# Kernel tuning notes

Hardware: AMD Instinct MI355X
Metric: run time of the kernel (lower is better)

## Reference

```python
import jax, jax.numpy as jnp
import numpy as np

GRID_LON = 17  # idx = lat*17 + lon in original code


def setup_inputs() -> dict:
    key = jax.random.key(0)
    ks = jax.random.split(key, 16)
    B, S, L = 512, 256, 64
    DIM_RHO, DIM_C, HID = 256, 128, 512
    N_LAT, N_LON = 17, GRID_LON

    rho = jax.random.normal(ks[0], (B, S, DIM_RHO), dtype=jnp.float32)
    c = jax.random.normal(ks[1], (1, DIM_C, N_LAT, N_LON), dtype=jnp.float32)
    w = jax.random.uniform(ks[2], (B, S), dtype=jnp.float32, minval=1e-3, maxval=1.0)
    l = jax.random.uniform(ks[3], (B,), dtype=jnp.float32, minval=0.1, maxval=10.0)
    roads = jax.random.randint(ks[4], (B, L), 0, N_LAT * N_LON)
    lon_idx = jax.random.randint(ks[5], (B, L), 0, N_LON)
    lat_idx = jax.random.randint(ks[6], (B, L), 0, N_LAT)

    sc = lambda fan_in: 1.0 / np.sqrt(fan_in)
    # f2: MLP(128, 256, 128) with selu
    f2_W1 = jax.random.uniform(ks[7], (DIM_C, 256), jnp.float32, -sc(DIM_C), sc(DIM_C))
    f2_b1 = jnp.zeros((256,), jnp.float32)
    f2_W2 = jax.random.uniform(ks[8], (256, DIM_C), jnp.float32, -sc(256), sc(256))
    f2_b2 = jnp.zeros((DIM_C,), jnp.float32)
    # f: MLP2(dim_rho + dim_c, hidden, 1) with selu (use_selu=True)
    fin = DIM_RHO + DIM_C
    f_W1 = jax.random.uniform(ks[9], (fin, HID), jnp.float32, -sc(fin), sc(fin))
    f_b1 = jnp.zeros((HID,), jnp.float32)
    f_W21 = jax.random.uniform(ks[10], (HID, 1), jnp.float32, -sc(HID), sc(HID))
    f_b21 = jnp.zeros((1,), jnp.float32)
    f_W22 = jax.random.uniform(ks[11], (HID, 1), jnp.float32, -sc(HID), sc(HID))
    f_b22 = jnp.zeros((1,), jnp.float32)

    return dict(rho=rho, c=c, w=w, l=l, roads=roads, lon_idx=lon_idx,
                lat_idx=lat_idx, f2_W1=f2_W1, f2_b1=f2_b1, f2_W2=f2_W2,
                f2_b2=f2_b2, f_W1=f_W1, f_b1=f_b1, f_W21=f_W21, f_b21=f_b21,
                f_W22=f_W22, f_b22=f_b22)


def reference(rho, c, w, l, roads, lon_idx, lat_idx,
              f2_W1, f2_b1, f2_W2, f2_b2,
              f_W1, f_b1, f_W21, f_b21, f_W22, f_b22):
    # c: (1, dim_c, n_lat, n_lon) -> (n_lat*n_lon, dim_c)
    c3 = jnp.squeeze(c, 0)                       # (dim_c, n_lat, n_lon)
    c_flat = jnp.transpose(c3, (1, 2, 0)).reshape(-1, c3.shape[0])  # (cells, dim_c)

    # ragged gather-mean, vectorized: (B, L) cell indices -> (B, dim_c)
    idx = lat_idx * GRID_LON + lon_idx           # (B, L)
    c_traj = jnp.mean(c_flat[idx], axis=1)       # (B, dim_c)

    # f2: selu MLP (dropout inactive / eval mode)
    h = jax.nn.selu(c_traj @ f2_W1 + f2_b1)
    c_tr = h @ f2_W2 + f2_b2                     # (B, dim_c)

    # broadcast over seq and concat with rho
    S = rho.shape[1]
    c_exp = jnp.broadcast_to(c_tr[:, None, :], (rho.shape[0], S, c_tr.shape[-1]))
    x = jnp.concatenate([rho, c_exp], axis=2)    # (B, S, dim_rho + dim_c)

    # f (MLP2, selu since use_selu=True)
    h1 = jax.nn.selu(x @ f_W1 + f_b1)            # (B, S, hidden)
    logm = (h1 @ f_W21 + f_b21)[..., 0]          # (B, S)
    logv = (h1 @ f_W22 + f_b22)[..., 0]          # (B, S)

    logw = jnp.log(w)
    logm_agg = jax.nn.logsumexp(logm + logw, axis=1)       # (B,)
    logv_agg = jax.nn.logsumexp(logv + 2.0 * logw, axis=1) # (B,)
    logl = jnp.log(l)
    log_mu = logl - logm_agg
    log_lambda = logl - 3.0 * logm_agg - logv_agg
    return (log_mu, log_lambda)
```

## Files before the change

### kernel.cpp

```cpp
#include <hip/hip_runtime.h>
#include <hip/hip_bf16.h>

typedef short bf16x8 __attribute__((ext_vector_type(8)));
typedef float f32x4 __attribute__((ext_vector_type(4)));
typedef _Float16 half4 __attribute__((ext_vector_type(4)));

__device__ __forceinline__ short f2bf(float f) {
    union { float f; unsigned u; } v; v.f = f;
    unsigned r = (v.u + 0x7FFFu + ((v.u >> 16) & 1u)) >> 16;
    return (short)r;
}

__device__ __forceinline__ float selu_f(float x) {
    const float scale = 1.0507009873554805f;
    const float sa = 1.0507009873554805f * 1.6732632423543772f;
    return x > 0.f ? scale * x : sa * (__expf(x) - 1.f);
}

__global__ void __launch_bounds__(512) prep_all_kernel(
    const float* __restrict__ c, const int* __restrict__ lat_idx,
    const int* __restrict__ lon_idx,
    const float* __restrict__ f2W1, const float* __restrict__ f2b1,
    const float* __restrict__ f2W2, const float* __restrict__ f2b2,
    const float* __restrict__ fW1, const float* __restrict__ fb1,
    const float* __restrict__ fW21, const float* __restrict__ fW22,
    short* __restrict__ w1img, _Float16* __restrict__ wvec,
    float* __restrict__ cbias)
{
    const int bid = blockIdx.x;
    const int t = threadIdx.x;

    if (bid < 512) {
        __shared__ int cells[64];
        __shared__ float ctraj[128];
        __shared__ float hbuf[256];
        __shared__ float ctrf[128];
        const int b = bid;

        if (t < 64) cells[t] = lat_idx[b * 64 + t] * 17 + lon_idx[b * 64 + t];
        __syncthreads();

        if (t < 128) {
            float s = 0.f;
            #pragma unroll 8
            for (int j = 0; j < 64; ++j) s += c[t * 289 + cells[j]];
            ctraj[t] = s * (1.f / 64.f);
        }
        __syncthreads();

        if (t < 256) {
            float acc = f2b1[t];
            #pragma unroll 8
            for (int i = 0; i < 128; ++i) acc += ctraj[i] * f2W1[i * 256 + t];
            hbuf[t] = selu_f(acc);
        }
        __syncthreads();

        if (t < 128) {
            float acc = f2b2[t];
            #pragma unroll 8
            for (int i = 0; i < 256; ++i) acc += hbuf[i] * f2W2[i * 128 + t];
            ctrf[t] = acc;
        }
        __syncthreads();

        float acc = fb1[t];
        #pragma unroll 8
        for (int i = 0; i < 128; ++i) acc += ctrf[i] * fW1[(256 + i) * 512 + t];
        cbias[b * 512 + t] = acc;
    } else if (bid < 768) {
        int I = (bid - 512) * 512 + t;
        int e = I & 7;
        int lane = (I >> 3) & 63;
        int cg = (I >> 9) & 31;
        int kc = I >> 14;
        int col = cg * 16 + (lane & 15);
        int k = kc * 32 + ((lane >> 4) << 3) + e;
        w1img[I] = f2bf(fW1[k * 512 + col]);
    } else {
        int I = (bid - 768) * 512 + t;
        int e = I & 3;
        int lane = (I >> 2) & 63;
        int nc = I >> 8;
        int l15 = lane & 15, hi = lane >> 4;
        int n = nc * 16 + hi * 4 + e;
        float v = (l15 == 0) ? fW21[n] : (l15 == 1 ? fW22[n] : 0.f);
        wvec[I] = (_Float16)v;
    }
}

__global__ void __launch_bounds__(512, 4) fused_gemm_kernel(
    const float* __restrict__ rho, const short* __restrict__ w1img,
    const float* __restrict__ cbias, const _Float16* __restrict__ wvec,
    float* __restrict__ plm, float* __restrict__ plv)
{
    __shared__ __align__(16) char smA[36864];

    const int tid  = threadIdx.x;
    const int lane = tid & 63;
    const int w    = tid >> 6;
    const int l15  = lane & 15;
    const int hi   = lane >> 4;

    const int b  = blockIdx.x >> 2;
    const int s0 = (blockIdx.x & 3) << 6;

    {
        const float* src = rho + (size_t)(b * 256 + s0) * 256 + tid * 8;
        const int kc_w = (tid >> 2) & 7;
        const int hi_w = tid & 3;
        const int sw_w = (tid >> 5) ^ (tid & 15);
        #pragma unroll
        for (int j = 0; j < 4; ++j) {
            float4 f0 = *(const float4*)(src + j * 4096);
            float4 f1 = *(const float4*)(src + j * 4096 + 4);
            union { bf16x8 h; unsigned u[4]; } pk;
            asm("v_cvt_pk_bf16_f32 %0, %1, %2" : "=v"(pk.u[0]) : "v"(f0.x), "v"(f0.y));
            asm("v_cvt_pk_bf16_f32 %0, %1, %2" : "=v"(pk.u[1]) : "v"(f0.z), "v"(f0.w));
            asm("v_cvt_pk_bf16_f32 %0, %1, %2" : "=v"(pk.u[2]) : "v"(f1.x), "v"(f1.y));
            asm("v_cvt_pk_bf16_f32 %0, %1, %2" : "=v"(pk.u[3]) : "v"(f1.z), "v"(f1.w));
            int slot = (kc_w * 4 + j) * 64 + hi_w * 16 + sw_w;
            *(bf16x8*)(smA + (slot << 4)) = pk.h;
        }
    }
    __syncthreads();

    f32x4 acc[4][4];
    #pragma unroll
    for (int nf = 0; nf < 4; ++nf)
        #pragma unroll
        for (int sf = 0; sf < 4; ++sf)
            acc[nf][sf] = (f32x4){0.f, 0.f, 0.f, 0.f};

    const char* bp = (const char*)w1img + w * 4096 + lane * 16;

    bf16x8 bN[4];
    #pragma unroll
    for (int nf = 0; nf < 4; ++nf)
        bN[nf] = *(const bf16x8*)(bp + nf * 1024);

    #pragma unroll
    for (int kc = 0; kc < 8; ++kc) {
        bf16x8 bC[4];
        #pragma unroll
        for (int nf = 0; nf < 4; ++nf) bC[nf] = bN[nf];
        if (kc < 7) {
            #pragma unroll
            for (int nf = 0; nf < 4; ++nf)
                bN[nf] = *(const bf16x8*)(bp + (size_t)(kc + 1) * 32768 + nf * 1024);
        }
        const int sw_r = l15 ^ (((kc & 3) << 2) | hi);
        const char* ab = smA + ((kc * 256 + hi * 16 + sw_r) << 4);
        bf16x8 aF[4];
        #pragma unroll
        for (int sf = 0; sf < 4; ++sf)
            aF[sf] = *(const bf16x8*)(ab + sf * 1024);
        #pragma unroll
        for (int nf = 0; nf < 4; ++nf)
            #pragma unroll
            for (int sf = 0; sf < 4; ++sf)
                acc[nf][sf] = __builtin_amdgcn_mfma_f32_16x16x32_bf16(
                    bC[nf], aF[sf], acc[nf][sf], 0, 0, 0);
    }

    f32x4 rd[4];
    #pragma unroll
    for (int sf = 0; sf < 4; ++sf) rd[sf] = (f32x4){0.f, 0.f, 0.f, 0.f};

    #pragma unroll
    for (int nf = 0; nf < 4; ++nf) {
        f32x4 cbf = *(const f32x4*)(cbias + b * 512 + w * 64 + nf * 16 + hi * 4);
        half4 wv = *(const half4*)(wvec + (size_t)(w * 4 + nf) * 256 + lane * 4);
        #pragma unroll
        for (int sf = 0; sf < 4; ++sf) {
            half4 pa;
            #pragma unroll
            for (int q = 0; q < 4; ++q)
                pa[q] = (_Float16)selu_f(acc[nf][sf][q] + cbf[q]);
            rd[sf] = __builtin_amdgcn_mfma_f32_16x16x16f16(pa, wv, rd[sf], 0, 0, 0);
        }
    }

    float* redM = (float*)(smA + 32768);
    float* redV = (float*)(smA + 34816);
    if (l15 == 0) {
        #pragma unroll
        for (int sf = 0; sf < 4; ++sf)
            *(f32x4*)&redM[w * 64 + sf * 16 + hi * 4] = rd[sf];
    } else if (l15 == 1) {
        #pragma unroll
        for (int sf = 0; sf < 4; ++sf)
            *(f32x4*)&redV[w * 64 + sf * 16 + hi * 4] = rd[sf];
    }

    __syncthreads();
    size_t obase = (size_t)b * 256 + s0;
    if (tid < 64) {
        float s = 0.f;
        #pragma unroll
        for (int j = 0; j < 8; ++j) s += redM[j * 64 + tid];
        plm[obase + tid] = s;
    } else if (tid < 128) {
        int rr = tid - 64;
        float s = 0.f;
        #pragma unroll
        for (int j = 0; j < 8; ++j) s += redV[j * 64 + rr];
        plv[obase + rr] = s;
    }
}

__global__ void __launch_bounds__(64) finalize_kernel(
    const float* __restrict__ plm, const float* __restrict__ plv,
    const float* __restrict__ w, const float* __restrict__ l,
    const float* __restrict__ b21p, const float* __restrict__ b22p,
    float* __restrict__ out)
{
    const int b = blockIdx.x;
    const int lane = threadIdx.x;
    const float b21 = b21p[0], b22 = b22p[0];

    float a1[4], a2[4];
    float m1 = -1e30f, m2 = -1e30f;
    #pragma unroll
    for (int i = 0; i < 4; ++i) {
        int s = i * 64 + lane;
        float lw = logf(w[b * 256 + s]);
        a1[i] = plm[b * 256 + s] + b21 + lw;
        a2[i] = plv[b * 256 + s] + b22 + 2.f * lw;
        m1 = fmaxf(m1, a1[i]);
        m2 = fmaxf(m2, a2[i]);
    }
    #pragma unroll
    for (int m = 1; m < 64; m <<= 1) {
        m1 = fmaxf(m1, __shfl_xor(m1, m));
        m2 = fmaxf(m2, __shfl_xor(m2, m));
    }
    float s1 = 0.f, s2 = 0.f;
    #pragma unroll
    for (int i = 0; i < 4; ++i) {
        s1 += expf(a1[i] - m1);
        s2 += expf(a2[i] - m2);
    }
    #pragma unroll
    for (int m = 1; m < 64; m <<= 1) {
        s1 += __shfl_xor(s1, m);
        s2 += __shfl_xor(s2, m);
    }
    if (lane == 0) {
        float lm_agg = m1 + logf(s1);
        float lv_agg = m2 + logf(s2);
        float logl = logf(l[b]);
        out[b]       = logl - lm_agg;
        out[512 + b] = logl - 3.f * lm_agg - lv_agg;
    }
}

extern "C" void kernel_launch(void* const* d_in, const int* in_sizes, int n_in,
                              void* d_out, int out_size, void* d_ws, size_t ws_size,
                              hipStream_t stream) {
    const float* rho     = (const float*)d_in[0];
    const float* c       = (const float*)d_in[1];
    const float* w       = (const float*)d_in[2];
    const float* l       = (const float*)d_in[3];
    const int*   lon_idx = (const int*)d_in[5];
    const int*   lat_idx = (const int*)d_in[6];
    const float* f2W1    = (const float*)d_in[7];
    const float* f2b1    = (const float*)d_in[8];
    const float* f2W2    = (const float*)d_in[9];
    const float* f2b2    = (const float*)d_in[10];
    const float* fW1     = (const float*)d_in[11];
    const float* fb1     = (const float*)d_in[12];
    const float* fW21    = (const float*)d_in[13];
    const float* fb21    = (const float*)d_in[14];
    const float* fW22    = (const float*)d_in[15];
    const float* fb22    = (const float*)d_in[16];
    float* out = (float*)d_out;

    char* ws = (char*)d_ws;
    float*     cbias = (float*)(ws);
    short*     w1img = (short*)(ws + 1048576);
    float*     plm   = (float*)(ws + 1310720);
    float*     plv   = (float*)(ws + 1835008);
    _Float16*  wvec  = (_Float16*)(ws + 2359296);

    prep_all_kernel<<<784, 512, 0, stream>>>(c, lat_idx, lon_idx,
                                             f2W1, f2b1, f2W2, f2b2,
                                             fW1, fb1, fW21, fW22,
                                             w1img, wvec, cbias);
    fused_gemm_kernel<<<2048, 512, 0, stream>>>(rho, w1img, cbias, wvec,
                                                plm, plv);
    finalize_kernel<<<512, 64, 0, stream>>>(plm, plv, w, l, fb21, fb22, out);
}
```

Before: 92.33 us.

## Stream W1 tiles via async global-to-LDS loads with triple buffering

Replaces the per-wave register prefetch of W1 fragments with direct global_load_lds transfers into a per-wave triple-buffered LDS region, issued two k-steps ahead and paced with explicit vmcnt waits. MFMA blocks are wrapped in s_setprio to favour the compute wave. LDS usage grows from 36 KB to 128 KB and launch bounds drop from 4 to 2 blocks per CU, so occupancy falls. The aim is to hide global load latency and free VGPRs, at the cost of extra LDS traffic.

```diff
diff --git a/kernel.cpp b/kernel.cpp
--- a/kernel.cpp
+++ b/kernel.cpp
@@ -15,6 +15,12 @@
     const float scale = 1.0507009873554805f;
     const float sa = 1.0507009873554805f * 1.6732632423543772f;
     return x > 0.f ? scale * x : sa * (__expf(x) - 1.f);
+}
+
+__device__ __forceinline__ void gld_lds16(const char* g, char* l) {
+    __builtin_amdgcn_global_load_lds(
+        (const __attribute__((address_space(1))) unsigned int*)g,
+        (__attribute__((address_space(3))) unsigned int*)l, 16, 0, 0);
 }
 
 __global__ void __launch_bounds__(512) prep_all_kernel(
@@ -89,12 +95,12 @@
     }
 }
 
-__global__ void __launch_bounds__(512, 4) fused_gemm_kernel(
+__global__ void __launch_bounds__(512, 2) fused_gemm_kernel(
     const float* __restrict__ rho, const short* __restrict__ w1img,
     const float* __restrict__ cbias, const _Float16* __restrict__ wvec,
     float* __restrict__ plm, float* __restrict__ plv)
 {
-    __shared__ __align__(16) char smA[36864];
+    __shared__ __align__(16) char smem[131072];
 
     const int tid  = threadIdx.x;
     const int lane = tid & 63;
@@ -104,6 +110,15 @@
 
     const int b  = blockIdx.x >> 2;
     const int s0 = (blockIdx.x & 3) << 6;
+
+    const char* bsrc = (const char*)w1img + w * 4096 + lane * 16;
+    char* bdst = smem + 32768 + w * 12288;
+
+    #pragma unroll
+    for (int j = 0; j < 4; ++j) gld_lds16(bsrc + j * 1024, bdst + j * 1024);
+    #pragma unroll
+    for (int j = 0; j < 4; ++j) gld_lds16(bsrc + 32768 + j * 1024,
+                                          bdst + 4096 + j * 1024);
 
     {
         const float* src = rho + (size_t)(b * 256 + s0) * 256 + tid * 8;
@@ -120,7 +135,7 @@
             asm("v_cvt_pk_bf16_f32 %0, %1, %2" : "=v"(pk.u[2]) : "v"(f1.x), "v"(f1.y));
             asm("v_cvt_pk_bf16_f32 %0, %1, %2" : "=v"(pk.u[3]) : "v"(f1.z), "v"(f1.w));
             int slot = (kc_w * 4 + j) * 64 + hi_w * 16 + sw_w;
-            *(bf16x8*)(smA + (slot << 4)) = pk.h;
+            *(bf16x8*)(smem + (slot << 4)) = pk.h;
         }
     }
     __syncthreads();
@@ -132,36 +147,50 @@
         for (int sf = 0; sf < 4; ++sf)
             acc[nf][sf] = (f32x4){0.f, 0.f, 0.f, 0.f};
 
-    const char* bp = (const char*)w1img + w * 4096 + lane * 16;
-
-    bf16x8 bN[4];
-    #pragma unroll
-    for (int nf = 0; nf < 4; ++nf)
-        bN[nf] = *(const bf16x8*)(bp + nf * 1024);
-
-    #pragma unroll
-    for (int kc = 0; kc < 8; ++kc) {
-        bf16x8 bC[4];
-        #pragma unroll
-        for (int nf = 0; nf < 4; ++nf) bC[nf] = bN[nf];
-        if (kc < 7) {
-            #pragma unroll
-            for (int nf = 0; nf < 4; ++nf)
-                bN[nf] = *(const bf16x8*)(bp + (size_t)(kc + 1) * 32768 + nf * 1024);
-        }
-        const int sw_r = l15 ^ (((kc & 3) << 2) | hi);
-        const char* ab = smA + ((kc * 256 + hi * 16 + sw_r) << 4);
-        bf16x8 aF[4];
-        #pragma unroll
-        for (int sf = 0; sf < 4; ++sf)
-            aF[sf] = *(const bf16x8*)(ab + sf * 1024);
-        #pragma unroll
-        for (int nf = 0; nf < 4; ++nf)
-            #pragma unroll
-            for (int sf = 0; sf < 4; ++sf)
-                acc[nf][sf] = __builtin_amdgcn_mfma_f32_16x16x32_bf16(
-                    bC[nf], aF[sf], acc[nf][sf], 0, 0, 0);
-    }
+#define KSTEP(KC, WAITASM)                                                     \
+    {                                                                          \
+        if ((KC) < 6) {                   \
+            const char* s_ = bsrc + ((KC) + 2) * 32768;                        \
+            char* d_ = bdst + (((KC) + 2) % 3) * 4096;                         \
+            gld_lds16(s_,          d_);                                        \
+            gld_lds16(s_ + 1024,   d_ + 1024);                                 \
+            gld_lds16(s_ + 2048,   d_ + 2048);                                 \
+            gld_lds16(s_ + 3072,   d_ + 3072);                                 \
+        }                                                                      \
+        asm volatile(WAITASM ::: "memory");                                    \
+        __builtin_amdgcn_sched_barrier(0);                                     \
+        {                                                                      \
+            const char* bb = bdst + ((KC) % 3) * 4096 + lane * 16;             \
+            bf16x8 bF[4];                                                      \
+            _Pragma("unroll")                                                  \
+            for (int nf = 0; nf < 4; ++nf)                                     \
+                bF[nf] = *(const bf16x8*)(bb + nf * 1024);                     \
+            const int sw_r = l15 ^ ((((KC) & 3) << 2) | hi);                   \
+            const char* ab = smem + (((KC) * 256 + hi * 16 + sw_r) << 4);      \
+            bf16x8 aF[4];                                                      \
+            _Pragma("unroll")                                                  \
+            for (int sf = 0; sf < 4; ++sf)                                     \
+                aF[sf] = *(const bf16x8*)(ab + sf * 1024);                     \
+            __builtin_amdgcn_s_setprio(1);                                     \
+            _Pragma("unroll")                                                  \
+            for (int nf = 0; nf < 4; ++nf)                                     \
+                _Pragma("unroll")                                              \
+                for (int sf = 0; sf < 4; ++sf)                                 \
+                    acc[nf][sf] = __builtin_amdgcn_mfma_f32_16x16x32_bf16(     \
+                        bF[nf], aF[sf], acc[nf][sf], 0, 0, 0);                 \
+            __builtin_amdgcn_s_setprio(0);                                     \
+        }                                                                      \
+    }
+
+    KSTEP(0, "s_waitcnt vmcnt(8)")
+    KSTEP(1, "s_waitcnt vmcnt(8)")
+    KSTEP(2, "s_waitcnt vmcnt(8)")
+    KSTEP(3, "s_waitcnt vmcnt(8)")
+    KSTEP(4, "s_waitcnt vmcnt(8)")
+    KSTEP(5, "s_waitcnt vmcnt(8)")
+    KSTEP(6, "s_waitcnt vmcnt(4)")
+    KSTEP(7, "s_waitcnt vmcnt(0)")
+#undef KSTEP
 
     f32x4 rd[4];
     #pragma unroll
@@ -181,8 +210,9 @@
         }
     }
 
-    float* redM = (float*)(smA + 32768);
-    float* redV = (float*)(smA + 34816);
+    __syncthreads();
+    float* redM = (float*)(smem + 32768);
+    float* redV = (float*)(smem + 34816);
     if (l15 == 0) {
         #pragma unroll
         for (int sf = 0; sf < 4; ++sf)
```

Result: slower. 109.9 us (+19.0%).

## Split GEMM N dimension across two blocks to raise occupancy

Applied to the files above, without the earlier changes.

Each GEMM block now computes only half of the 512 hidden columns, which halves the accumulator registers and allows a higher occupancy launch bound. Twice as many blocks are launched. Each writes partial logm/logv sums to separate buffers, and the finalize kernel adds them. In exchange, every rho tile is loaded and converted to bf16 twice, which relies on adjacent blocks hitting in cache.

```diff
diff --git a/kernel.cpp b/kernel.cpp
--- a/kernel.cpp
+++ b/kernel.cpp
@@ -89,10 +89,10 @@
     }
 }
 
-__global__ void __launch_bounds__(512, 4) fused_gemm_kernel(
+__global__ void __launch_bounds__(512, 6) fused_gemm_kernel(
     const float* __restrict__ rho, const short* __restrict__ w1img,
     const float* __restrict__ cbias, const _Float16* __restrict__ wvec,
-    float* __restrict__ plm, float* __restrict__ plv)
+    float* __restrict__ plmP, float* __restrict__ plvP)
 {
     __shared__ __align__(16) char smA[36864];
 
@@ -102,8 +102,9 @@
     const int l15  = lane & 15;
     const int hi   = lane >> 4;
 
-    const int b  = blockIdx.x >> 2;
-    const int s0 = (blockIdx.x & 3) << 6;
+    const int b  = blockIdx.x >> 3;
+    const int s0 = ((blockIdx.x >> 1) & 3) << 6;
+    const int nh = blockIdx.x & 1;
 
     {
         const float* src = rho + (size_t)(b * 256 + s0) * 256 + tid * 8;
@@ -125,30 +126,20 @@
     }
     __syncthreads();
 
-    f32x4 acc[4][4];
-    #pragma unroll
-    for (int nf = 0; nf < 4; ++nf)
+    f32x4 acc[2][4];
+    #pragma unroll
+    for (int nf = 0; nf < 2; ++nf)
         #pragma unroll
         for (int sf = 0; sf < 4; ++sf)
             acc[nf][sf] = (f32x4){0.f, 0.f, 0.f, 0.f};
 
-    const char* bp = (const char*)w1img + w * 4096 + lane * 16;
-
-    bf16x8 bN[4];
-    #pragma unroll
-    for (int nf = 0; nf < 4; ++nf)
-        bN[nf] = *(const bf16x8*)(bp + nf * 1024);
+    const char* bp = (const char*)w1img + (nh * 16 + w * 2) * 1024 + lane * 16;
 
     #pragma unroll
     for (int kc = 0; kc < 8; ++kc) {
-        bf16x8 bC[4];
-        #pragma unroll
-        for (int nf = 0; nf < 4; ++nf) bC[nf] = bN[nf];
-        if (kc < 7) {
-            #pragma unroll
-            for (int nf = 0; nf < 4; ++nf)
-                bN[nf] = *(const bf16x8*)(bp + (size_t)(kc + 1) * 32768 + nf * 1024);
-        }
+        bf16x8 bC[2];
+        bC[0] = *(const bf16x8*)(bp + (size_t)kc * 32768);
+        bC[1] = *(const bf16x8*)(bp + (size_t)kc * 32768 + 1024);
         const int sw_r = l15 ^ (((kc & 3) << 2) | hi);
         const char* ab = smA + ((kc * 256 + hi * 16 + sw_r) << 4);
         bf16x8 aF[4];
@@ -156,7 +147,7 @@
         for (int sf = 0; sf < 4; ++sf)
             aF[sf] = *(const bf16x8*)(ab + sf * 1024);
         #pragma unroll
-        for (int nf = 0; nf < 4; ++nf)
+        for (int nf = 0; nf < 2; ++nf)
             #pragma unroll
             for (int sf = 0; sf < 4; ++sf)
                 acc[nf][sf] = __builtin_amdgcn_mfma_f32_16x16x32_bf16(
@@ -168,9 +159,10 @@
     for (int sf = 0; sf < 4; ++sf) rd[sf] = (f32x4){0.f, 0.f, 0.f, 0.f};
 
     #pragma unroll
-    for (int nf = 0; nf < 4; ++nf) {
-        f32x4 cbf = *(const f32x4*)(cbias + b * 512 + w * 64 + nf * 16 + hi * 4);
-        half4 wv = *(const half4*)(wvec + (size_t)(w * 4 + nf) * 256 + lane * 4);
+    for (int nf = 0; nf < 2; ++nf) {
+        const int nc = nh * 16 + w * 2 + nf;
+        f32x4 cbf = *(const f32x4*)(cbias + b * 512 + nc * 16 + hi * 4);
+        half4 wv = *(const half4*)(wvec + (size_t)nc * 256 + lane * 4);
         #pragma unroll
         for (int sf = 0; sf < 4; ++sf) {
             half4 pa;
@@ -194,23 +186,23 @@
     }
 
     __syncthreads();
-    size_t obase = (size_t)b * 256 + s0;
+    size_t obase = (size_t)nh * 131072 + (size_t)b * 256 + s0;
     if (tid < 64) {
         float s = 0.f;
         #pragma unroll
         for (int j = 0; j < 8; ++j) s += redM[j * 64 + tid];
-        plm[obase + tid] = s;
+        plmP[obase + tid] = s;
     } else if (tid < 128) {
         int rr = tid - 64;
         float s = 0.f;
         #pragma unroll
         for (int j = 0; j < 8; ++j) s += redV[j * 64 + rr];
-        plv[obase + rr] = s;
+        plvP[obase + rr] = s;
     }
 }
 
 __global__ void __launch_bounds__(64) finalize_kernel(
-    const float* __restrict__ plm, const float* __restrict__ plv,
+    const float* __restrict__ plmP, const float* __restrict__ plvP,
     const float* __restrict__ w, const float* __restrict__ l,
     const float* __restrict__ b21p, const float* __restrict__ b22p,
     float* __restrict__ out)
@@ -224,9 +216,10 @@
     #pragma unroll
     for (int i = 0; i < 4; ++i) {
         int s = i * 64 + lane;
-        float lw = logf(w[b * 256 + s]);
-        a1[i] = plm[b * 256 + s] + b21 + lw;
-        a2[i] = plv[b * 256 + s] + b22 + 2.f * lw;
+        int idx = b * 256 + s;
+        float lw = logf(w[idx]);
+        a1[i] = plmP[idx] + plmP[131072 + idx] + b21 + lw;
+        a2[i] = plvP[idx] + plvP[131072 + idx] + b22 + 2.f * lw;
         m1 = fmaxf(m1, a1[i]);
         m2 = fmaxf(m2, a2[i]);
     }
@@ -279,15 +272,15 @@
     char* ws = (char*)d_ws;
     float*     cbias = (float*)(ws);
     short*     w1img = (short*)(ws + 1048576);
-    float*     plm   = (float*)(ws + 1310720);
-    float*     plv   = (float*)(ws + 1835008);
-    _Float16*  wvec  = (_Float16*)(ws + 2359296);
+    float*     plmP  = (float*)(ws + 1310720);
+    float*     plvP  = (float*)(ws + 2359296);
+    _Float16*  wvec  = (_Float16*)(ws + 3407872);
 
     prep_all_kernel<<<784, 512, 0, stream>>>(c, lat_idx, lon_idx,
                                              f2W1, f2b1, f2W2, f2b2,
                                              fW1, fb1, fW21, fW22,
                                              w1img, wvec, cbias);
-    fused_gemm_kernel<<<2048, 512, 0, stream>>>(rho, w1img, cbias, wvec,
-                                                plm, plv);
-    finalize_kernel<<<512, 64, 0, stream>>>(plm, plv, w, l, fb21, fb22, out);
-}
+    fused_gemm_kernel<<<4096, 512, 0, stream>>>(rho, w1img, cbias, wvec,
+                                                plmP, plvP);
+    finalize_kernel<<<512, 64, 0, stream>>>(plmP, plvP, w, l, fb21, fb22, out);
+}
```

Result: slower. 98.08 us (+6.2%).

## Switch main GEMM to 32x32x16 MFMA and do head projection with scalar FMAs

Applied to the files above, without the earlier changes.

The fused GEMM now uses 32x32x16 bf16 MFMA tiles instead of 16x16x32, so each wave does 4 larger MFMAs per k-step with a new XOR-swizzled LDS layout and a matching weight image. The second-layer projection (two output heads) moves from an f16 MFMA onto per-lane FMAs in fp32. Each lane writes partial sums to a larger LDS reduction buffer. This drops the separate wvec prep blocks and the f16 rounding of activations, and aims for better MFMA throughput and fewer LDS reads per FLOP. The cost is more VALU work in the epilogue and a 16-way reduction instead of 8-way.

```diff
diff --git a/kernel.cpp b/kernel.cpp
--- a/kernel.cpp
+++ b/kernel.cpp
@@ -3,7 +3,7 @@
 
 typedef short bf16x8 __attribute__((ext_vector_type(8)));
 typedef float f32x4 __attribute__((ext_vector_type(4)));
-typedef _Float16 half4 __attribute__((ext_vector_type(4)));
+typedef float f32x16 __attribute__((ext_vector_type(16)));
 
 __device__ __forceinline__ short f2bf(float f) {
     union { float f; unsigned u; } v; v.f = f;
@@ -23,9 +23,7 @@
     const float* __restrict__ f2W1, const float* __restrict__ f2b1,
     const float* __restrict__ f2W2, const float* __restrict__ f2b2,
     const float* __restrict__ fW1, const float* __restrict__ fb1,
-    const float* __restrict__ fW21, const float* __restrict__ fW22,
-    short* __restrict__ w1img, _Float16* __restrict__ wvec,
-    float* __restrict__ cbias)
+    short* __restrict__ w1img, float* __restrict__ cbias)
 {
     const int bid = blockIdx.x;
     const int t = threadIdx.x;
@@ -68,129 +66,115 @@
         #pragma unroll 8
         for (int i = 0; i < 128; ++i) acc += ctrf[i] * fW1[(256 + i) * 512 + t];
         cbias[b * 512 + t] = acc;
-    } else if (bid < 768) {
+    } else {
         int I = (bid - 512) * 512 + t;
         int e = I & 7;
         int lane = (I >> 3) & 63;
-        int cg = (I >> 9) & 31;
-        int kc = I >> 14;
-        int col = cg * 16 + (lane & 15);
-        int k = kc * 32 + ((lane >> 4) << 3) + e;
+        int ng = (I >> 9) & 15;
+        int kk = I >> 13;
+        int k = kk * 16 + ((lane >> 5) << 3) + e;
+        int col = ng * 32 + (lane & 31);
         w1img[I] = f2bf(fW1[k * 512 + col]);
-    } else {
-        int I = (bid - 768) * 512 + t;
-        int e = I & 3;
-        int lane = (I >> 2) & 63;
-        int nc = I >> 8;
-        int l15 = lane & 15, hi = lane >> 4;
-        int n = nc * 16 + hi * 4 + e;
-        float v = (l15 == 0) ? fW21[n] : (l15 == 1 ? fW22[n] : 0.f);
-        wvec[I] = (_Float16)v;
     }
 }
 
 __global__ void __launch_bounds__(512, 4) fused_gemm_kernel(
     const float* __restrict__ rho, const short* __restrict__ w1img,
-    const float* __restrict__ cbias, const _Float16* __restrict__ wvec,
+    const float* __restrict__ cbias, const float* __restrict__ fw21,
+    const float* __restrict__ fw22,
     float* __restrict__ plm, float* __restrict__ plv)
 {
-    __shared__ __align__(16) char smA[36864];
+    __shared__ __align__(16) char smA[40960];
 
     const int tid  = threadIdx.x;
     const int lane = tid & 63;
     const int w    = tid >> 6;
-    const int l15  = lane & 15;
-    const int hi   = lane >> 4;
+    const int l31  = lane & 31;
+    const int h    = lane >> 5;
 
     const int b  = blockIdx.x >> 2;
     const int s0 = (blockIdx.x & 3) << 6;
 
     {
         const float* src = rho + (size_t)(b * 256 + s0) * 256 + tid * 8;
-        const int kc_w = (tid >> 2) & 7;
-        const int hi_w = tid & 3;
-        const int sw_w = (tid >> 5) ^ (tid & 15);
+        const int kk_w = (tid & 31) >> 1;
+        const int h_w  = tid & 1;
+        const int xw   = (kk_w & 7) << 4;
         #pragma unroll
         for (int j = 0; j < 4; ++j) {
             float4 f0 = *(const float4*)(src + j * 4096);
             float4 f1 = *(const float4*)(src + j * 4096 + 4);
-            union { bf16x8 h; unsigned u[4]; } pk;
+            union { bf16x8 hh; unsigned u[4]; } pk;
             asm("v_cvt_pk_bf16_f32 %0, %1, %2" : "=v"(pk.u[0]) : "v"(f0.x), "v"(f0.y));
             asm("v_cvt_pk_bf16_f32 %0, %1, %2" : "=v"(pk.u[1]) : "v"(f0.z), "v"(f0.w));
             asm("v_cvt_pk_bf16_f32 %0, %1, %2" : "=v"(pk.u[2]) : "v"(f1.x), "v"(f1.y));
             asm("v_cvt_pk_bf16_f32 %0, %1, %2" : "=v"(pk.u[3]) : "v"(f1.z), "v"(f1.w));
-            int slot = (kc_w * 4 + j) * 64 + hi_w * 16 + sw_w;
-            *(bf16x8*)(smA + (slot << 4)) = pk.h;
+            int si_w = j >> 1;
+            int ld   = (h_w << 5) | ((j & 1) * 16 + (tid >> 5));
+            int byte = ((((kk_w * 2 + si_w) * 64) + ld) << 4) ^ xw;
+            *(bf16x8*)(smA + byte) = pk.hh;
         }
     }
     __syncthreads();
 
-    f32x4 acc[4][4];
-    #pragma unroll
-    for (int nf = 0; nf < 4; ++nf)
-        #pragma unroll
-        for (int sf = 0; sf < 4; ++sf)
-            acc[nf][sf] = (f32x4){0.f, 0.f, 0.f, 0.f};
-
-    const char* bp = (const char*)w1img + w * 4096 + lane * 16;
-
-    bf16x8 bN[4];
-    #pragma unroll
-    for (int nf = 0; nf < 4; ++nf)
-        bN[nf] = *(const bf16x8*)(bp + nf * 1024);
-
-    #pragma unroll
-    for (int kc = 0; kc < 8; ++kc) {
-        bf16x8 bC[4];
-        #pragma unroll
-        for (int nf = 0; nf < 4; ++nf) bC[nf] = bN[nf];
-        if (kc < 7) {
+    f32x16 acc[2][2];
+    #pragma unroll
+    for (int si = 0; si < 2; ++si)
+        #pragma unroll
+        for (int ni = 0; ni < 2; ++ni)
+            acc[si][ni] = (f32x16)(0.f);
+
+    const char* bp = (const char*)w1img + ((w * 2) * 64 + lane) * 16;
+
+    bf16x8 wN0 = *(const bf16x8*)(bp);
+    bf16x8 wN1 = *(const bf16x8*)(bp + 1024);
+
+    #pragma unroll
+    for (int kk = 0; kk < 16; ++kk) {
+        bf16x8 wC0 = wN0, wC1 = wN1;
+        if (kk < 15) {
+            wN0 = *(const bf16x8*)(bp + (size_t)(kk + 1) * 16384);
+            wN1 = *(const bf16x8*)(bp + (size_t)(kk + 1) * 16384 + 1024);
+        }
+        const int xr = (kk & 7) << 4;
+        const int base = (((kk * 2) * 64 + lane) << 4) ^ xr;
+        bf16x8 aF0 = *(const bf16x8*)(smA + base);
+        bf16x8 aF1 = *(const bf16x8*)(smA + base + 1024);
+        acc[0][0] = __builtin_amdgcn_mfma_f32_32x32x16_bf16(wC0, aF0, acc[0][0], 0, 0, 0);
+        acc[0][1] = __builtin_amdgcn_mfma_f32_32x32x16_bf16(wC1, aF0, acc[0][1], 0, 0, 0);
+        acc[1][0] = __builtin_amdgcn_mfma_f32_32x32x16_bf16(wC0, aF1, acc[1][0], 0, 0, 0);
+        acc[1][1] = __builtin_amdgcn_mfma_f32_32x32x16_bf16(wC1, aF1, acc[1][1], 0, 0, 0);
+    }
+
+    float mm0 = 0.f, mm1 = 0.f, vv0 = 0.f, vv1 = 0.f;
+    #pragma unroll
+    for (int ni = 0; ni < 2; ++ni) {
+        #pragma unroll
+        for (int q = 0; q < 4; ++q) {
+            int n0 = w * 64 + ni * 32 + 8 * q + 4 * h;
+            f32x4 cb  = *(const f32x4*)(cbias + b * 512 + n0);
+            f32x4 w1r = *(const f32x4*)(fw21 + n0);
+            f32x4 w2r = *(const f32x4*)(fw22 + n0);
             #pragma unroll
-            for (int nf = 0; nf < 4; ++nf)
-                bN[nf] = *(const bf16x8*)(bp + (size_t)(kc + 1) * 32768 + nf * 1024);
-        }
-        const int sw_r = l15 ^ (((kc & 3) << 2) | hi);
-        const char* ab = smA + ((kc * 256 + hi * 16 + sw_r) << 4);
-        bf16x8 aF[4];
-        #pragma unroll
-        for (int sf = 0; sf < 4; ++sf)
-            aF[sf] = *(const bf16x8*)(ab + sf * 1024);
-        #pragma unroll
-        for (int nf = 0; nf < 4; ++nf)
-            #pragma unroll
-            for (int sf = 0; sf < 4; ++sf)
-                acc[nf][sf] = __builtin_amdgcn_mfma_f32_16x16x32_bf16(
-                    bC[nf], aF[sf], acc[nf][sf], 0, 0, 0);
-    }
-
-    f32x4 rd[4];
-    #pragma unroll
-    for (int sf = 0; sf < 4; ++sf) rd[sf] = (f32x4){0.f, 0.f, 0.f, 0.f};
-
-    #pragma unroll
-    for (int nf = 0; nf < 4; ++nf) {
-        f32x4 cbf = *(const f32x4*)(cbias + b * 512 + w * 64 + nf * 16 + hi * 4);
-        half4 wv = *(const half4*)(wvec + (size_t)(w * 4 + nf) * 256 + lane * 4);
-        #pragma unroll
-        for (int sf = 0; sf < 4; ++sf) {
-            half4 pa;
-            #pragma unroll
-            for (int q = 0; q < 4; ++q)
-                pa[q] = (_Float16)selu_f(acc[nf][sf][q] + cbf[q]);
-            rd[sf] = __builtin_amdgcn_mfma_f32_16x16x16f16(pa, wv, rd[sf], 0, 0, 0);
+            for (int e = 0; e < 4; ++e) {
+                float sA = selu_f(acc[0][ni][4 * q + e] + cb[e]);
+                float sB = selu_f(acc[1][ni][4 * q + e] + cb[e]);
+                mm0 += sA * w1r[e];
+                vv0 += sA * w2r[e];
+                mm1 += sB * w1r[e];
+                vv1 += sB * w2r[e];
+            }
         }
     }
 
     float* redM = (float*)(smA + 32768);
-    float* redV = (float*)(smA + 34816);
-    if (l15 == 0) {
-        #pragma unroll
-        for (int sf = 0; sf < 4; ++sf)
-            *(f32x4*)&redM[w * 64 + sf * 16 + hi * 4] = rd[sf];
-    } else if (l15 == 1) {
-        #pragma unroll
-        for (int sf = 0; sf < 4; ++sf)
-            *(f32x4*)&redV[w * 64 + sf * 16 + hi * 4] = rd[sf];
+    float* redV = (float*)(smA + 36864);
+    {
+        int idx = (w * 2 + h) * 64;
+        redM[idx + l31]      = mm0;
+        redM[idx + 32 + l31] = mm1;
+        redV[idx + l31]      = vv0;
+        redV[idx + 32 + l31] = vv1;
     }
 
     __syncthreads();
@@ -198,13 +182,13 @@
     if (tid < 64) {
         float s = 0.f;
         #pragma unroll
-        for (int j = 0; j < 8; ++j) s += redM[j * 64 + tid];
+        for (int j = 0; j < 16; ++j) s += redM[j * 64 + tid];
         plm[obase + tid] = s;
     } else if (tid < 128) {
         int rr = tid - 64;
         float s = 0.f;
         #pragma unroll
-        for (int j = 0; j < 8; ++j) s += redV[j * 64 + rr];
+        for (int j = 0; j < 16; ++j) s += redV[j * 64 + rr];
         plv[obase + rr] = s;
     }
 }
@@ -281,13 +265,11 @@
     short*     w1img = (short*)(ws + 1048576);
     float*     plm   = (float*)(ws + 1310720);
     float*     plv   = (float*)(ws + 1835008);
-    _Float16*  wvec  = (_Float16*)(ws + 2359296);
-
-    prep_all_kernel<<<784, 512, 0, stream>>>(c, lat_idx, lon_idx,
+
+    prep_all_kernel<<<768, 512, 0, stream>>>(c, lat_idx, lon_idx,
                                              f2W1, f2b1, f2W2, f2b2,
-                                             fW1, fb1, fW21, fW22,
-                                             w1img, wvec, cbias);
-    fused_gemm_kernel<<<2048, 512, 0, stream>>>(rho, w1img, cbias, wvec,
+                                             fW1, fb1, w1img, cbias);
+    fused_gemm_kernel<<<2048, 512, 0, stream>>>(rho, w1img, cbias, fW21, fW22,
                                                 plm, plv);
     finalize_kernel<<<512, 64, 0, stream>>>(plm, plv, w, l, fb21, fb22, out);
 }
```

Result: slower. 113.8 us (+23.3%).
